# Performance work log

Hardware: AMD Instinct MI355X
Metric: run time of the kernel (lower is better)

Reference implementation:

```python
import jax, jax.numpy as jnp
import numpy as np

N_NODES = 100000
N_EDGES = 1600000
N_GRAPHS = 256
IN_F = 64   # global_features (GNN input dim)
OUT_F = 64  # node_features (GNN output dim)


def setup_inputs() -> dict:
    key = jax.random.key(0)
    ks = jax.random.split(key, 8)
    x = jax.random.normal(ks[0], (N_NODES, IN_F), dtype=jnp.float32)
    edge_index = jax.random.randint(ks[1], (2, N_EDGES), 0, N_NODES, dtype=jnp.int64)
    batch = jnp.sort(jax.random.randint(ks[2], (N_NODES,), 0, N_GRAPHS, dtype=jnp.int64))
    # GNNLayer linear: in=global_features, out=node_features
    W_gnn = jax.random.normal(ks[3], (IN_F, OUT_F), dtype=jnp.float32) / np.sqrt(IN_F)
    b_gnn = jnp.zeros((OUT_F,), dtype=jnp.float32)
    # global_attention: Linear(node_features, 1)
    W_att = jax.random.normal(ks[4], (OUT_F, 1), dtype=jnp.float32) / np.sqrt(OUT_F)
    b_att = jnp.zeros((1,), dtype=jnp.float32)
    return {"x": x, "edge_index": edge_index, "batch": batch,
            "W_gnn": W_gnn, "b_gnn": b_gnn, "W_att": W_att, "b_att": b_att}


def reference(x, edge_index, batch, W_gnn, b_gnn, W_att, b_att):
    src, dst = edge_index[0], edge_index[1]
    # --- GNN message passing layer: aggregate neighbor features, transform ---
    agg = jax.ops.segment_sum(x[src], dst, num_segments=N_NODES)  # [N, IN_F]
    h = jax.nn.relu((x + agg) @ W_gnn + b_gnn)                    # [N, OUT_F]
    # --- attention scores + scatter softmax over batch segments ---
    scores = (h @ W_att + b_att)[:, 0]                            # [N]
    seg_max = jax.ops.segment_max(scores, batch, num_segments=N_GRAPHS)
    e = jnp.exp(scores - seg_max[batch])
    denom = jax.ops.segment_sum(e, batch, num_segments=N_GRAPHS)
    w = e / denom[batch]                                          # [N]
    # --- weighted scatter-add pooling ---
    out = jax.ops.segment_sum(w[:, None] * h, batch, num_segments=N_GRAPHS)
    return out  # [N_GRAPHS, OUT_F]
```

## Files before the change

### kernel.cpp

```cpp
#include <hip/hip_runtime.h>

#define N_NODES  100000
#define N_EDGES  1600000
#define N_GRAPHS 256
#define F        64


#define CHUNK    8192
#define NCHUNK   196
#define NBUCK    391
#define BCAP     5120

#define CAST_ELEMS   (N_NODES * F / 4)
#define CAST_BLOCKS  ((CAST_ELEMS + 1023) / 1024)
#define BC_BLOCKS    (NCHUNK + CAST_BLOCKS)

__device__ __forceinline__ unsigned short f2bf(float f) {
    unsigned int u = __float_as_uint(f);
    u += 0x7FFFu + ((u >> 16) & 1u);
    return (unsigned short)(u >> 16);
}

__global__ __launch_bounds__(256) void zero_kernel(
        int* __restrict__ balloc, float* __restrict__ out,
        float* __restrict__ denom) {
    int i = blockIdx.x * 256 + threadIdx.x;
    if (i < NBUCK) balloc[i] = 0;
    if (i < N_GRAPHS * F) out[i] = 0.f;
    if (i < N_GRAPHS) denom[i] = 0.f;
}

__global__ __launch_bounds__(1024) void bin_cast_kernel(
        const int* __restrict__ src, const int* __restrict__ dst,
        const float* __restrict__ x, unsigned short* __restrict__ xh,
        unsigned int* __restrict__ pairs, int* __restrict__ balloc) {
    int tid = threadIdx.x;
    int b   = blockIdx.x;

    if (b >= NCHUNK) {
        int i = (b - NCHUNK) * 1024 + tid;
        if (i < CAST_ELEMS) {
            float4 v = ((const float4*)x)[i];
            ushort4 o;
            o.x = f2bf(v.x); o.y = f2bf(v.y); o.z = f2bf(v.z); o.w = f2bf(v.w);
            ((ushort4*)xh)[i] = o;
        }
        return;
    }

    __shared__ int hist[NBUCK];
    __shared__ int roffs[NBUCK];
    __shared__ int curs[NBUCK];
    __shared__ int bbase[NBUCK];
    __shared__ int wsum[16];
    __shared__ unsigned int   stage[CHUNK];
    __shared__ unsigned short bstage[CHUNK];

    int base = b * CHUNK;
    int m    = min(CHUNK, N_EDGES - base);
    int lane = tid & 63;
    int wv   = tid >> 6;

    for (int k = tid; k < NBUCK; k += 1024) hist[k] = 0;
    __syncthreads();

    int de[8], se[8];
    #pragma unroll
    for (int r = 0; r < 8; ++r) {
        int e = tid + r * 1024;
        if (e < m) {
            de[r] = dst[base + e];
            se[r] = src[base + e];
            atomicAdd(&hist[de[r] >> 8], 1);
        } else {
            de[r] = -1; se[r] = 0;
        }
    }
    __syncthreads();

    int v = (tid < NBUCK) ? hist[tid] : 0;
    #pragma unroll
    for (int o = 1; o < 64; o <<= 1) {
        int u = __shfl_up(v, o, 64);
        if (lane >= o) v += u;
    }
    if (lane == 63) wsum[wv] = v;
    __syncthreads();
    if (tid < 16) {
        int s = wsum[tid];
        #pragma unroll
        for (int o = 1; o < 16; o <<= 1) {
            int u = __shfl_up(s, o, 64);
            if (tid >= o) s += u;
        }
        wsum[tid] = s;
    }
    __syncthreads();
    if (wv > 0) v += wsum[wv - 1];
    if (tid < NBUCK) {
        int excl = v - hist[tid];
        roffs[tid] = excl;
        curs[tid]  = excl;
        if (hist[tid] > 0)
            bbase[tid] = tid * BCAP + atomicAdd(&balloc[tid], hist[tid]);
    }
    __syncthreads();

    #pragma unroll
    for (int r = 0; r < 8; ++r) {
        if (de[r] >= 0) {
            int bk  = de[r] >> 8;
            int pos = atomicAdd(&curs[bk], 1);
            stage[pos]  = ((unsigned)(de[r] & 255) << 17) | (unsigned)se[r];
            bstage[pos] = (unsigned short)bk;
        }
    }
    __syncthreads();

    for (int e = tid; e < m; e += 1024) {
        int bk = bstage[e];
        pairs[bbase[bk] + (e - roffs[bk])] = stage[e];
    }
}

__global__ __launch_bounds__(512) void bucket_sort_kernel(
        unsigned int* __restrict__ pairs,
        const int* __restrict__ balloc,
        int* __restrict__ nbeg, int* __restrict__ nend) {
    __shared__ int hist[256];
    __shared__ int roffs[256];
    __shared__ int curs[256];
    __shared__ int wsum[8];
    __shared__ int sorted[BCAP];

    int tid   = threadIdx.x;
    int b     = blockIdx.x;
    int lane  = tid & 63;
    int wv    = tid >> 6;
    int node0 = b << 8;
    int nn    = min(256, N_NODES - node0);
    int E     = balloc[b];
    int base  = b * BCAP;

    for (int k = tid; k < 256; k += 512) hist[k] = 0;
    __syncthreads();
    for (int i = tid; i < E; i += 512)
        atomicAdd(&hist[pairs[base + i] >> 17], 1);
    __syncthreads();

    int c = (tid < 256) ? hist[tid] : 0;
    int v = c;
    #pragma unroll
    for (int o = 1; o < 64; o <<= 1) {
        int u = __shfl_up(v, o, 64);
        if (lane >= o) v += u;
    }
    if (tid < 256 && lane == 63) wsum[wv] = v;
    __syncthreads();
    if (tid < 4) {
        int s = wsum[tid];
        int u = __shfl_up(s, 1, 64); if (tid >= 1) s += u;
        u     = __shfl_up(s, 2, 64); if (tid >= 2) s += u;
        wsum[tid] = s;
    }
    __syncthreads();
    if (tid < 256) {
        if (wv > 0) v += wsum[wv - 1];
        int excl = v - c;
        roffs[tid] = excl;
        curs[tid]  = excl;
        if (tid < nn) {
            nbeg[node0 + tid] = base + excl;
            nend[node0 + tid] = base + excl + c;
        }
    }
    __syncthreads();

    for (int i = tid; i < E; i += 512) {
        unsigned int p = pairs[base + i];
        int pos = atomicAdd(&curs[p >> 17], 1);
        sorted[pos] = (int)(p & 0x1FFFFu);
    }
    __syncthreads();
    for (int i = tid; i < E; i += 512)
        pairs[base + i] = (unsigned int)sorted[i];
}

#define NODES_PER_WAVE 25
#define GT_NWAVES  (N_NODES / NODES_PER_WAVE)
#define GT_BLOCKS  (GT_NWAVES / 4)

__device__ __forceinline__ float bfl(unsigned int u) { return __uint_as_float(u << 16); }
__device__ __forceinline__ float bfh(unsigned int u) { return __uint_as_float(u & 0xFFFF0000u); }

__global__ __launch_bounds__(256) void gather_pool_kernel(
        const unsigned short* __restrict__ xh,
        const int*   __restrict__ nbeg,
        const int*   __restrict__ nend,
        const int*   __restrict__ eidx,
        const int*   __restrict__ batch,
        const float* __restrict__ Wg,
        const float* __restrict__ bg,
        const float* __restrict__ Wa,
        const float* __restrict__ ba,
        float*       __restrict__ out_acc,
        float*       __restrict__ denom) {
    int tid  = threadIdx.x;
    int lane = tid & 63;
    int grp  = lane >> 3;
    int c    = lane & 7;
    int waveId = blockIdx.x * 4 + (tid >> 6);

    int n0   = waveId * NODES_PER_WAVE;
    int nEnd = n0 + NODES_PER_WAVE;

    float wcol[F];
    #pragma unroll
    for (int k = 0; k < F; ++k) wcol[k] = Wg[k * F + lane];
    float bgl = bg[lane];
    float wal = Wa[lane];
    float ba0 = ba[0];

    const uint4* xh4 = (const uint4*)xh;

    int   cur_g = batch[n0];
    float accw  = 0.f;
    float denw  = 0.f;

    int pb = nbeg[n0];
    int pe = nend[n0];
    int sl_cur = (pb + lane < pe) ? eidx[pb + lane] : 0;

    for (int n = n0; n < nEnd; ++n) {
        int start = pb, end = pe;
        int sl    = sl_cur;
        if (n + 1 < nEnd) {
            pb = nbeg[n + 1];
            pe = nend[n + 1];
            sl_cur = (pb + lane < pe) ? eidx[pb + lane] : 0;
        }

        float a0=0.f,a1=0.f,a2=0.f,a3=0.f,a4=0.f,a5=0.f,a6=0.f,a7=0.f;
        {
            int jmax = end - start; if (jmax > 64) jmax = 64;
            for (int j = 0; j < jmax; j += 8) {
                int el = j + grp;
                int s  = __shfl(sl, el, 64);
                if (el < jmax) {
                    uint4 v = xh4[s * 8 + c];
                    a0 += bfl(v.x); a1 += bfh(v.x);
                    a2 += bfl(v.y); a3 += bfh(v.y);
                    a4 += bfl(v.z); a5 += bfh(v.z);
                    a6 += bfl(v.w); a7 += bfh(v.w);
                }
            }
        }
        for (int base = start + 64; base < end; base += 64) {
            int jmax = end - base; if (jmax > 64) jmax = 64;
            int sl2 = (base + lane < end) ? eidx[base + lane] : 0;
            for (int j = 0; j < jmax; j += 8) {
                int el = j + grp;
                int s  = __shfl(sl2, el, 64);
                if (el < jmax) {
                    uint4 v = xh4[s * 8 + c];
                    a0 += bfl(v.x); a1 += bfh(v.x);
                    a2 += bfl(v.y); a3 += bfh(v.y);
                    a4 += bfl(v.z); a5 += bfh(v.z);
                    a6 += bfl(v.w); a7 += bfh(v.w);
                }
            }
        }
        #pragma unroll
        for (int o = 8; o <= 32; o <<= 1) {
            a0 += __shfl_xor(a0, o, 64); a1 += __shfl_xor(a1, o, 64);
            a2 += __shfl_xor(a2, o, 64); a3 += __shfl_xor(a3, o, 64);
            a4 += __shfl_xor(a4, o, 64); a5 += __shfl_xor(a5, o, 64);
            a6 += __shfl_xor(a6, o, 64); a7 += __shfl_xor(a7, o, 64);
        }
        {
            uint4 v = xh4[n * 8 + c];
            a0 += bfl(v.x); a1 += bfh(v.x);
            a2 += bfl(v.y); a3 += bfh(v.y);
            a4 += bfl(v.z); a5 += bfh(v.z);
            a6 += bfl(v.w); a7 += bfh(v.w);
        }

        float re[8] = {a0,a1,a2,a3,a4,a5,a6,a7};
        float q0=0.f,q1=0.f,q2=0.f,q3=0.f,q4=0.f,q5=0.f,q6=0.f,q7=0.f;
        #pragma unroll
        for (int k = 0; k < F; k += 8) {
            int ln = k >> 3;
            q0 += __int_as_float(__builtin_amdgcn_readlane(__float_as_int(re[0]), ln)) * wcol[k + 0];
            q1 += __int_as_float(__builtin_amdgcn_readlane(__float_as_int(re[1]), ln)) * wcol[k + 1];
            q2 += __int_as_float(__builtin_amdgcn_readlane(__float_as_int(re[2]), ln)) * wcol[k + 2];
            q3 += __int_as_float(__builtin_amdgcn_readlane(__float_as_int(re[3]), ln)) * wcol[k + 3];
            q4 += __int_as_float(__builtin_amdgcn_readlane(__float_as_int(re[4]), ln)) * wcol[k + 4];
            q5 += __int_as_float(__builtin_amdgcn_readlane(__float_as_int(re[5]), ln)) * wcol[k + 5];
            q6 += __int_as_float(__builtin_amdgcn_readlane(__float_as_int(re[6]), ln)) * wcol[k + 6];
            q7 += __int_as_float(__builtin_amdgcn_readlane(__float_as_int(re[7]), ln)) * wcol[k + 7];
        }
        float hv = ((q0 + q1) + (q2 + q3)) + ((q4 + q5) + (q6 + q7)) + bgl;
        hv = hv > 0.f ? hv : 0.f;

        float p = hv * wal;
        #pragma unroll
        for (int o = 32; o > 0; o >>= 1)
            p += __shfl_down(p, o, 64);
        float s = __int_as_float(__builtin_amdgcn_readlane(__float_as_int(p), 0)) + ba0;
        float e = __expf(s);

        int g = batch[n];
        if (g != cur_g) {
            atomicAdd(&out_acc[cur_g * F + lane], accw);
            if (lane == 0) atomicAdd(&denom[cur_g], denw);
            accw = 0.f; denw = 0.f; cur_g = g;
        }
        accw += e * hv;
        denw += e;
    }
    atomicAdd(&out_acc[cur_g * F + lane], accw);
    if (lane == 0) atomicAdd(&denom[cur_g], denw);
}

__global__ __launch_bounds__(256) void finalize_kernel(
        float* __restrict__ out, const float* __restrict__ denom) {
    int i = blockIdx.x * 256 + threadIdx.x;
    if (i >= N_GRAPHS * F) return;
    float d = denom[i >> 6];
    out[i] = (d > 0.f) ? out[i] / d : 0.f;
}

extern "C" void kernel_launch(void* const* d_in, const int* in_sizes, int n_in,
                              void* d_out, int out_size, void* d_ws, size_t ws_size,
                              hipStream_t stream) {
    const float* x     = (const float*)d_in[0];
    const int*   ei    = (const int*)d_in[1];
    const int*   batch = (const int*)d_in[2];
    const float* Wg    = (const float*)d_in[3];
    const float* bg    = (const float*)d_in[4];
    const float* Wa    = (const float*)d_in[5];
    const float* ba    = (const float*)d_in[6];
    float* out = (float*)d_out;

    const int* src = ei;
    const int* dst = ei + N_EDGES;

    char* ws = (char*)d_ws;
    unsigned short* xh     = (unsigned short*)(ws);
    unsigned int*   pairs  = (unsigned int*)(ws + 12800000);
    int*            nbeg   = (int*)(ws + 20807680);
    int*            nend   = (int*)(ws + 21207808);
    int*            balloc = (int*)(ws + 21607936);
    float*          denom  = (float*)(ws + 21610240);

    zero_kernel       <<<64, 256, 0, stream>>>(balloc, out, denom);
    bin_cast_kernel   <<<BC_BLOCKS, 1024, 0, stream>>>(src, dst, x, xh, pairs, balloc);
    bucket_sort_kernel<<<NBUCK, 512, 0, stream>>>(pairs, balloc, nbeg, nend);
    gather_pool_kernel<<<GT_BLOCKS, 256, 0, stream>>>(
        xh, nbeg, nend, (const int*)pairs, batch, Wg, bg, Wa, ba, out, denom);
    finalize_kernel   <<<(N_GRAPHS * F + 255) / 256, 256, 0, stream>>>(out, denom);
}
```

Baseline: 179.3 us.

## Move GNN weights to packed-bf16 shared memory and halve nodes per wave

The per-lane 64-float weight column held in registers is replaced by a bf16-packed copy of W_gnn in shared memory, read inside the matvec loop. This lowers register pressure, and nodes per wave drop from 25 to 13 so more waves run in parallel. The zero kernel is folded into the cast blocks plus a memset, which removes one launch. The costs are extra LDS reads per node, a per-block weight conversion, and bf16 rounding of the weights.

```diff
diff --git a/kernel.cpp b/kernel.cpp
--- a/kernel.cpp
+++ b/kernel.cpp
@@ -21,23 +21,19 @@
     return (unsigned short)(u >> 16);
 }
 
-__global__ __launch_bounds__(256) void zero_kernel(
-        int* __restrict__ balloc, float* __restrict__ out,
-        float* __restrict__ denom) {
-    int i = blockIdx.x * 256 + threadIdx.x;
-    if (i < NBUCK) balloc[i] = 0;
-    if (i < N_GRAPHS * F) out[i] = 0.f;
-    if (i < N_GRAPHS) denom[i] = 0.f;
-}
-
 __global__ __launch_bounds__(1024) void bin_cast_kernel(
         const int* __restrict__ src, const int* __restrict__ dst,
         const float* __restrict__ x, unsigned short* __restrict__ xh,
-        unsigned int* __restrict__ pairs, int* __restrict__ balloc) {
+        unsigned int* __restrict__ pairs, int* __restrict__ balloc,
+        float* __restrict__ out, float* __restrict__ denom) {
     int tid = threadIdx.x;
     int b   = blockIdx.x;
 
     if (b >= NCHUNK) {
+        if (b == NCHUNK) {
+            for (int i = tid; i < N_GRAPHS * F; i += 1024) out[i] = 0.f;
+            if (tid < N_GRAPHS) denom[tid] = 0.f;
+        }
         int i = (b - NCHUNK) * 1024 + tid;
         if (i < CAST_ELEMS) {
             float4 v = ((const float4*)x)[i];
@@ -186,9 +182,9 @@
         pairs[base + i] = (unsigned int)sorted[i];
 }
 
-#define NODES_PER_WAVE 25
-#define GT_NWAVES  (N_NODES / NODES_PER_WAVE)
-#define GT_BLOCKS  (GT_NWAVES / 4)
+#define NODES_PER_WAVE 13
+#define GT_NWAVES  ((N_NODES + NODES_PER_WAVE - 1) / NODES_PER_WAVE)
+#define GT_BLOCKS  ((GT_NWAVES + 3) / 4)
 
 __device__ __forceinline__ float bfl(unsigned int u) { return __uint_as_float(u << 16); }
 __device__ __forceinline__ float bfh(unsigned int u) { return __uint_as_float(u & 0xFFFF0000u); }
@@ -205,18 +201,25 @@
         const float* __restrict__ ba,
         float*       __restrict__ out_acc,
         float*       __restrict__ denom) {
+    __shared__ unsigned int shw[32 * 64];
+
     int tid  = threadIdx.x;
     int lane = tid & 63;
+    for (int i = tid; i < 32 * 64; i += 256) {
+        int kk = i >> 6, f = i & 63;
+        unsigned int lo = (unsigned int)f2bf(Wg[(2 * kk)     * F + f]);
+        unsigned int hi = (unsigned int)f2bf(Wg[(2 * kk + 1) * F + f]);
+        shw[i] = lo | (hi << 16);
+    }
+    __syncthreads();
+
     int grp  = lane >> 3;
     int c    = lane & 7;
     int waveId = blockIdx.x * 4 + (tid >> 6);
-
     int n0   = waveId * NODES_PER_WAVE;
-    int nEnd = n0 + NODES_PER_WAVE;
-
-    float wcol[F];
-    #pragma unroll
-    for (int k = 0; k < F; ++k) wcol[k] = Wg[k * F + lane];
+    if (n0 >= N_NODES) return;
+    int nEnd = min(n0 + NODES_PER_WAVE, N_NODES);
+
     float bgl = bg[lane];
     float wal = Wa[lane];
     float ba0 = ba[0];
@@ -255,9 +258,9 @@
                 }
             }
         }
-        for (int base = start + 64; base < end; base += 64) {
-            int jmax = end - base; if (jmax > 64) jmax = 64;
-            int sl2 = (base + lane < end) ? eidx[base + lane] : 0;
+        for (int base2 = start + 64; base2 < end; base2 += 64) {
+            int jmax = end - base2; if (jmax > 64) jmax = 64;
+            int sl2 = (base2 + lane < end) ? eidx[base2 + lane] : 0;
             for (int j = 0; j < jmax; j += 8) {
                 int el = j + grp;
                 int s  = __shfl(sl2, el, 64);
@@ -288,16 +291,23 @@
         float re[8] = {a0,a1,a2,a3,a4,a5,a6,a7};
         float q0=0.f,q1=0.f,q2=0.f,q3=0.f,q4=0.f,q5=0.f,q6=0.f,q7=0.f;
         #pragma unroll
-        for (int k = 0; k < F; k += 8) {
-            int ln = k >> 3;
-            q0 += __int_as_float(__builtin_amdgcn_readlane(__float_as_int(re[0]), ln)) * wcol[k + 0];
-            q1 += __int_as_float(__builtin_amdgcn_readlane(__float_as_int(re[1]), ln)) * wcol[k + 1];
-            q2 += __int_as_float(__builtin_amdgcn_readlane(__float_as_int(re[2]), ln)) * wcol[k + 2];
-            q3 += __int_as_float(__builtin_amdgcn_readlane(__float_as_int(re[3]), ln)) * wcol[k + 3];
-            q4 += __int_as_float(__builtin_amdgcn_readlane(__float_as_int(re[4]), ln)) * wcol[k + 4];
-            q5 += __int_as_float(__builtin_amdgcn_readlane(__float_as_int(re[5]), ln)) * wcol[k + 5];
-            q6 += __int_as_float(__builtin_amdgcn_readlane(__float_as_int(re[6]), ln)) * wcol[k + 6];
-            q7 += __int_as_float(__builtin_amdgcn_readlane(__float_as_int(re[7]), ln)) * wcol[k + 7];
+        for (int kk8 = 0; kk8 < 8; ++kk8) {
+            float y0 = __int_as_float(__builtin_amdgcn_readlane(__float_as_int(re[0]), kk8));
+            float y1 = __int_as_float(__builtin_amdgcn_readlane(__float_as_int(re[1]), kk8));
+            float y2 = __int_as_float(__builtin_amdgcn_readlane(__float_as_int(re[2]), kk8));
+            float y3 = __int_as_float(__builtin_amdgcn_readlane(__float_as_int(re[3]), kk8));
+            float y4 = __int_as_float(__builtin_amdgcn_readlane(__float_as_int(re[4]), kk8));
+            float y5 = __int_as_float(__builtin_amdgcn_readlane(__float_as_int(re[5]), kk8));
+            float y6 = __int_as_float(__builtin_amdgcn_readlane(__float_as_int(re[6]), kk8));
+            float y7 = __int_as_float(__builtin_amdgcn_readlane(__float_as_int(re[7]), kk8));
+            unsigned int u0 = shw[(4 * kk8 + 0) * 64 + lane];
+            unsigned int u1 = shw[(4 * kk8 + 1) * 64 + lane];
+            unsigned int u2 = shw[(4 * kk8 + 2) * 64 + lane];
+            unsigned int u3 = shw[(4 * kk8 + 3) * 64 + lane];
+            q0 += y0 * bfl(u0); q1 += y1 * bfh(u0);
+            q2 += y2 * bfl(u1); q3 += y3 * bfh(u1);
+            q4 += y4 * bfl(u2); q5 += y5 * bfh(u2);
+            q6 += y6 * bfl(u3); q7 += y7 * bfh(u3);
         }
         float hv = ((q0 + q1) + (q2 + q3)) + ((q4 + q5) + (q6 + q7)) + bgl;
         hv = hv > 0.f ? hv : 0.f;
@@ -322,7 +332,7 @@
     if (lane == 0) atomicAdd(&denom[cur_g], denw);
 }
 
-__global__ __launch_bounds__(256) void finalize_kernel(
+__global__ __launch_bounds__(256) void fin_kernel(
         float* __restrict__ out, const float* __restrict__ denom) {
     int i = blockIdx.x * 256 + threadIdx.x;
     if (i >= N_GRAPHS * F) return;
@@ -353,10 +363,11 @@
     int*            balloc = (int*)(ws + 21607936);
     float*          denom  = (float*)(ws + 21610240);
 
-    zero_kernel       <<<64, 256, 0, stream>>>(balloc, out, denom);
-    bin_cast_kernel   <<<BC_BLOCKS, 1024, 0, stream>>>(src, dst, x, xh, pairs, balloc);
+    hipMemsetAsync(balloc, 0, NBUCK * sizeof(int), stream);
+    bin_cast_kernel   <<<BC_BLOCKS, 1024, 0, stream>>>(src, dst, x, xh, pairs,
+                                                       balloc, out, denom);
     bucket_sort_kernel<<<NBUCK, 512, 0, stream>>>(pairs, balloc, nbeg, nend);
     gather_pool_kernel<<<GT_BLOCKS, 256, 0, stream>>>(
         xh, nbeg, nend, (const int*)pairs, batch, Wg, bg, Wa, ba, out, denom);
-    finalize_kernel   <<<(N_GRAPHS * F + 255) / 256, 256, 0, stream>>>(out, denom);
-}
+    fin_kernel        <<<64, 256, 0, stream>>>(out, denom);
+}
```

New measurement: 193.6 us. +8.0%, slower.

## Fuse bucket sort, gather-pool and finalize into one kernel with last-block finalize

Applied to the files above, without the earlier changes.

Merges the per-bucket counting sort with the gather/transform/pool stage so that sorted edge lists and node offsets stay in shared memory instead of being written back to global memory and reread. Each 1024-thread block handles 256 nodes, 16 per wave. The final normalization runs in whichever block finishes last, detected with a global done counter. The zeroing of out/denom moves into the cast blocks and a memset, removing three launches. The trade-off is fewer, larger blocks (391 blocks of 16 waves, versus 1000 blocks of 4 waves before), which may lower parallelism and latency hiding in the gather phase.

```diff
diff --git a/kernel.cpp b/kernel.cpp
--- a/kernel.cpp
+++ b/kernel.cpp
@@ -20,24 +20,22 @@
     u += 0x7FFFu + ((u >> 16) & 1u);
     return (unsigned short)(u >> 16);
 }
-
-__global__ __launch_bounds__(256) void zero_kernel(
-        int* __restrict__ balloc, float* __restrict__ out,
-        float* __restrict__ denom) {
-    int i = blockIdx.x * 256 + threadIdx.x;
-    if (i < NBUCK) balloc[i] = 0;
-    if (i < N_GRAPHS * F) out[i] = 0.f;
-    if (i < N_GRAPHS) denom[i] = 0.f;
-}
+__device__ __forceinline__ float bfl(unsigned int u) { return __uint_as_float(u << 16); }
+__device__ __forceinline__ float bfh(unsigned int u) { return __uint_as_float(u & 0xFFFF0000u); }
 
 __global__ __launch_bounds__(1024) void bin_cast_kernel(
         const int* __restrict__ src, const int* __restrict__ dst,
         const float* __restrict__ x, unsigned short* __restrict__ xh,
-        unsigned int* __restrict__ pairs, int* __restrict__ balloc) {
+        unsigned int* __restrict__ pairs, int* __restrict__ balloc,
+        float* __restrict__ out, float* __restrict__ denom) {
     int tid = threadIdx.x;
     int b   = blockIdx.x;
 
     if (b >= NCHUNK) {
+        if (b == NCHUNK) {
+            for (int i = tid; i < N_GRAPHS * F; i += 1024) out[i] = 0.f;
+            if (tid < N_GRAPHS) denom[tid] = 0.f;
+        }
         int i = (b - NCHUNK) * 1024 + tid;
         if (i < CAST_ELEMS) {
             float4 v = ((const float4*)x)[i];
@@ -123,28 +121,38 @@
     }
 }
 
-__global__ __launch_bounds__(512) void bucket_sort_kernel(
-        unsigned int* __restrict__ pairs,
-        const int* __restrict__ balloc,
-        int* __restrict__ nbeg, int* __restrict__ nend) {
+__global__ __launch_bounds__(1024) void sort_gather_kernel(
+        const unsigned short* __restrict__ xh,
+        const unsigned int* __restrict__ pairs,
+        const int*   __restrict__ balloc,
+        const int*   __restrict__ batch,
+        const float* __restrict__ Wg,
+        const float* __restrict__ bg,
+        const float* __restrict__ Wa,
+        const float* __restrict__ ba,
+        float*       __restrict__ out,
+        float*       __restrict__ denom,
+        unsigned int* __restrict__ done) {
     __shared__ int hist[256];
-    __shared__ int roffs[256];
     __shared__ int curs[256];
-    __shared__ int wsum[8];
+    __shared__ int lbeg[256];
+    __shared__ int lend[256];
+    __shared__ int wsum[4];
     __shared__ int sorted[BCAP];
-
-    int tid   = threadIdx.x;
-    int b     = blockIdx.x;
-    int lane  = tid & 63;
-    int wv    = tid >> 6;
+    __shared__ int lastFlag;
+
+    int tid  = threadIdx.x;
+    int b    = blockIdx.x;
+    int lane = tid & 63;
+    int wv   = tid >> 6;
     int node0 = b << 8;
     int nn    = min(256, N_NODES - node0);
     int E     = balloc[b];
     int base  = b * BCAP;
 
-    for (int k = tid; k < 256; k += 512) hist[k] = 0;
-    __syncthreads();
-    for (int i = tid; i < E; i += 512)
+    if (tid < 256) hist[tid] = 0;
+    __syncthreads();
+    for (int i = tid; i < E; i += 1024)
         atomicAdd(&hist[pairs[base + i] >> 17], 1);
     __syncthreads();
 
@@ -167,52 +175,21 @@
     if (tid < 256) {
         if (wv > 0) v += wsum[wv - 1];
         int excl = v - c;
-        roffs[tid] = excl;
-        curs[tid]  = excl;
-        if (tid < nn) {
-            nbeg[node0 + tid] = base + excl;
-            nend[node0 + tid] = base + excl + c;
-        }
-    }
-    __syncthreads();
-
-    for (int i = tid; i < E; i += 512) {
+        curs[tid] = excl;
+        lbeg[tid] = excl;
+        lend[tid] = excl + c;
+    }
+    __syncthreads();
+
+    for (int i = tid; i < E; i += 1024) {
         unsigned int p = pairs[base + i];
         int pos = atomicAdd(&curs[p >> 17], 1);
         sorted[pos] = (int)(p & 0x1FFFFu);
     }
     __syncthreads();
-    for (int i = tid; i < E; i += 512)
-        pairs[base + i] = (unsigned int)sorted[i];
-}
-
-#define NODES_PER_WAVE 25
-#define GT_NWAVES  (N_NODES / NODES_PER_WAVE)
-#define GT_BLOCKS  (GT_NWAVES / 4)
-
-__device__ __forceinline__ float bfl(unsigned int u) { return __uint_as_float(u << 16); }
-__device__ __forceinline__ float bfh(unsigned int u) { return __uint_as_float(u & 0xFFFF0000u); }
-
-__global__ __launch_bounds__(256) void gather_pool_kernel(
-        const unsigned short* __restrict__ xh,
-        const int*   __restrict__ nbeg,
-        const int*   __restrict__ nend,
-        const int*   __restrict__ eidx,
-        const int*   __restrict__ batch,
-        const float* __restrict__ Wg,
-        const float* __restrict__ bg,
-        const float* __restrict__ Wa,
-        const float* __restrict__ ba,
-        float*       __restrict__ out_acc,
-        float*       __restrict__ denom) {
-    int tid  = threadIdx.x;
-    int lane = tid & 63;
-    int grp  = lane >> 3;
-    int c    = lane & 7;
-    int waveId = blockIdx.x * 4 + (tid >> 6);
-
-    int n0   = waveId * NODES_PER_WAVE;
-    int nEnd = n0 + NODES_PER_WAVE;
+
+    int grp = lane >> 3;
+    int cc  = lane & 7;
 
     float wcol[F];
     #pragma unroll
@@ -223,111 +200,126 @@
 
     const uint4* xh4 = (const uint4*)xh;
 
-    int   cur_g = batch[n0];
-    float accw  = 0.f;
-    float denw  = 0.f;
-
-    int pb = nbeg[n0];
-    int pe = nend[n0];
-    int sl_cur = (pb + lane < pe) ? eidx[pb + lane] : 0;
-
-    for (int n = n0; n < nEnd; ++n) {
-        int start = pb, end = pe;
-        int sl    = sl_cur;
-        if (n + 1 < nEnd) {
-            pb = nbeg[n + 1];
-            pe = nend[n + 1];
-            sl_cur = (pb + lane < pe) ? eidx[pb + lane] : 0;
-        }
-
-        float a0=0.f,a1=0.f,a2=0.f,a3=0.f,a4=0.f,a5=0.f,a6=0.f,a7=0.f;
-        {
-            int jmax = end - start; if (jmax > 64) jmax = 64;
-            for (int j = 0; j < jmax; j += 8) {
-                int el = j + grp;
-                int s  = __shfl(sl, el, 64);
-                if (el < jmax) {
-                    uint4 v = xh4[s * 8 + c];
-                    a0 += bfl(v.x); a1 += bfh(v.x);
-                    a2 += bfl(v.y); a3 += bfh(v.y);
-                    a4 += bfl(v.z); a5 += bfh(v.z);
-                    a6 += bfl(v.w); a7 += bfh(v.w);
+    int nl0 = wv * 16;
+    int myn = nn - nl0; if (myn > 16) myn = 16;
+
+    if (myn > 0) {
+        int   cur_g = batch[node0 + nl0];
+        float accw  = 0.f;
+        float denw  = 0.f;
+
+        int pb = lbeg[nl0];
+        int pe = lend[nl0];
+        int sl_cur = (pb + lane < pe) ? sorted[pb + lane] : 0;
+
+        for (int q = 0; q < myn; ++q) {
+            int n = node0 + nl0 + q;
+            int start = pb, end = pe;
+            int sl    = sl_cur;
+            if (q + 1 < myn) {
+                pb = lbeg[nl0 + q + 1];
+                pe = lend[nl0 + q + 1];
+                sl_cur = (pb + lane < pe) ? sorted[pb + lane] : 0;
+            }
+
+            float a0=0.f,a1=0.f,a2=0.f,a3=0.f,a4=0.f,a5=0.f,a6=0.f,a7=0.f;
+            {
+                int jmax = end - start; if (jmax > 64) jmax = 64;
+                for (int j = 0; j < jmax; j += 8) {
+                    int el = j + grp;
+                    int s  = __shfl(sl, el, 64);
+                    if (el < jmax) {
+                        uint4 vv = xh4[s * 8 + cc];
+                        a0 += bfl(vv.x); a1 += bfh(vv.x);
+                        a2 += bfl(vv.y); a3 += bfh(vv.y);
+                        a4 += bfl(vv.z); a5 += bfh(vv.z);
+                        a6 += bfl(vv.w); a7 += bfh(vv.w);
+                    }
                 }
             }
-        }
-        for (int base = start + 64; base < end; base += 64) {
-            int jmax = end - base; if (jmax > 64) jmax = 64;
-            int sl2 = (base + lane < end) ? eidx[base + lane] : 0;
-            for (int j = 0; j < jmax; j += 8) {
-                int el = j + grp;
-                int s  = __shfl(sl2, el, 64);
-                if (el < jmax) {
-                    uint4 v = xh4[s * 8 + c];
-                    a0 += bfl(v.x); a1 += bfh(v.x);
-                    a2 += bfl(v.y); a3 += bfh(v.y);
-                    a4 += bfl(v.z); a5 += bfh(v.z);
-                    a6 += bfl(v.w); a7 += bfh(v.w);
+            for (int b2 = start + 64; b2 < end; b2 += 64) {
+                int jmax = end - b2; if (jmax > 64) jmax = 64;
+                int sl2 = (b2 + lane < end) ? sorted[b2 + lane] : 0;
+                for (int j = 0; j < jmax; j += 8) {
+                    int el = j + grp;
+                    int s  = __shfl(sl2, el, 64);
+                    if (el < jmax) {
+                        uint4 vv = xh4[s * 8 + cc];
+                        a0 += bfl(vv.x); a1 += bfh(vv.x);
+                        a2 += bfl(vv.y); a3 += bfh(vv.y);
+                        a4 += bfl(vv.z); a5 += bfh(vv.z);
+                        a6 += bfl(vv.w); a7 += bfh(vv.w);
+                    }
                 }
             }
-        }
-        #pragma unroll
-        for (int o = 8; o <= 32; o <<= 1) {
-            a0 += __shfl_xor(a0, o, 64); a1 += __shfl_xor(a1, o, 64);
-            a2 += __shfl_xor(a2, o, 64); a3 += __shfl_xor(a3, o, 64);
-            a4 += __shfl_xor(a4, o, 64); a5 += __shfl_xor(a5, o, 64);
-            a6 += __shfl_xor(a6, o, 64); a7 += __shfl_xor(a7, o, 64);
-        }
-        {
-            uint4 v = xh4[n * 8 + c];
-            a0 += bfl(v.x); a1 += bfh(v.x);
-            a2 += bfl(v.y); a3 += bfh(v.y);
-            a4 += bfl(v.z); a5 += bfh(v.z);
-            a6 += bfl(v.w); a7 += bfh(v.w);
-        }
-
-        float re[8] = {a0,a1,a2,a3,a4,a5,a6,a7};
-        float q0=0.f,q1=0.f,q2=0.f,q3=0.f,q4=0.f,q5=0.f,q6=0.f,q7=0.f;
-        #pragma unroll
-        for (int k = 0; k < F; k += 8) {
-            int ln = k >> 3;
-            q0 += __int_as_float(__builtin_amdgcn_readlane(__float_as_int(re[0]), ln)) * wcol[k + 0];
-            q1 += __int_as_float(__builtin_amdgcn_readlane(__float_as_int(re[1]), ln)) * wcol[k + 1];
-            q2 += __int_as_float(__builtin_amdgcn_readlane(__float_as_int(re[2]), ln)) * wcol[k + 2];
-            q3 += __int_as_float(__builtin_amdgcn_readlane(__float_as_int(re[3]), ln)) * wcol[k + 3];
-            q4 += __int_as_float(__builtin_amdgcn_readlane(__float_as_int(re[4]), ln)) * wcol[k + 4];
-            q5 += __int_as_float(__builtin_amdgcn_readlane(__float_as_int(re[5]), ln)) * wcol[k + 5];
-            q6 += __int_as_float(__builtin_amdgcn_readlane(__float_as_int(re[6]), ln)) * wcol[k + 6];
-            q7 += __int_as_float(__builtin_amdgcn_readlane(__float_as_int(re[7]), ln)) * wcol[k + 7];
-        }
-        float hv = ((q0 + q1) + (q2 + q3)) + ((q4 + q5) + (q6 + q7)) + bgl;
-        hv = hv > 0.f ? hv : 0.f;
-
-        float p = hv * wal;
-        #pragma unroll
-        for (int o = 32; o > 0; o >>= 1)
-            p += __shfl_down(p, o, 64);
-        float s = __int_as_float(__builtin_amdgcn_readlane(__float_as_int(p), 0)) + ba0;
-        float e = __expf(s);
-
-        int g = batch[n];
-        if (g != cur_g) {
-            atomicAdd(&out_acc[cur_g * F + lane], accw);
-            if (lane == 0) atomicAdd(&denom[cur_g], denw);
-            accw = 0.f; denw = 0.f; cur_g = g;
-        }
-        accw += e * hv;
-        denw += e;
-    }
-    atomicAdd(&out_acc[cur_g * F + lane], accw);
-    if (lane == 0) atomicAdd(&denom[cur_g], denw);
-}
-
-__global__ __launch_bounds__(256) void finalize_kernel(
-        float* __restrict__ out, const float* __restrict__ denom) {
-    int i = blockIdx.x * 256 + threadIdx.x;
-    if (i >= N_GRAPHS * F) return;
-    float d = denom[i >> 6];
-    out[i] = (d > 0.f) ? out[i] / d : 0.f;
+            #pragma unroll
+            for (int o = 8; o <= 32; o <<= 1) {
+                a0 += __shfl_xor(a0, o, 64); a1 += __shfl_xor(a1, o, 64);
+                a2 += __shfl_xor(a2, o, 64); a3 += __shfl_xor(a3, o, 64);
+                a4 += __shfl_xor(a4, o, 64); a5 += __shfl_xor(a5, o, 64);
+                a6 += __shfl_xor(a6, o, 64); a7 += __shfl_xor(a7, o, 64);
+            }
+            {
+                uint4 vv = xh4[n * 8 + cc];
+                a0 += bfl(vv.x); a1 += bfh(vv.x);
+                a2 += bfl(vv.y); a3 += bfh(vv.y);
+                a4 += bfl(vv.z); a5 += bfh(vv.z);
+                a6 += bfl(vv.w); a7 += bfh(vv.w);
+            }
+
+            float re[8] = {a0,a1,a2,a3,a4,a5,a6,a7};
+            float q0=0.f,q1=0.f,q2=0.f,q3=0.f,q4=0.f,q5=0.f,q6=0.f,q7=0.f;
+            #pragma unroll
+            for (int k = 0; k < F; k += 8) {
+                int ln = k >> 3;
+                q0 += __int_as_float(__builtin_amdgcn_readlane(__float_as_int(re[0]), ln)) * wcol[k + 0];
+                q1 += __int_as_float(__builtin_amdgcn_readlane(__float_as_int(re[1]), ln)) * wcol[k + 1];
+                q2 += __int_as_float(__builtin_amdgcn_readlane(__float_as_int(re[2]), ln)) * wcol[k + 2];
+                q3 += __int_as_float(__builtin_amdgcn_readlane(__float_as_int(re[3]), ln)) * wcol[k + 3];
+                q4 += __int_as_float(__builtin_amdgcn_readlane(__float_as_int(re[4]), ln)) * wcol[k + 4];
+                q5 += __int_as_float(__builtin_amdgcn_readlane(__float_as_int(re[5]), ln)) * wcol[k + 5];
+                q6 += __int_as_float(__builtin_amdgcn_readlane(__float_as_int(re[6]), ln)) * wcol[k + 6];
+                q7 += __int_as_float(__builtin_amdgcn_readlane(__float_as_int(re[7]), ln)) * wcol[k + 7];
+            }
+            float hv = ((q0 + q1) + (q2 + q3)) + ((q4 + q5) + (q6 + q7)) + bgl;
+            hv = hv > 0.f ? hv : 0.f;
+
+            float p = hv * wal;
+            #pragma unroll
+            for (int o = 32; o > 0; o >>= 1)
+                p += __shfl_down(p, o, 64);
+            float s = __int_as_float(__builtin_amdgcn_readlane(__float_as_int(p), 0)) + ba0;
+            float e = __expf(s);
+
+            int g = batch[n];
+            if (g != cur_g) {
+                atomicAdd(&out[cur_g * F + lane], accw);
+                if (lane == 0) atomicAdd(&denom[cur_g], denw);
+                accw = 0.f; denw = 0.f; cur_g = g;
+            }
+            accw += e * hv;
+            denw += e;
+        }
+        atomicAdd(&out[cur_g * F + lane], accw);
+        if (lane == 0) atomicAdd(&denom[cur_g], denw);
+    }
+
+    __threadfence();
+    __syncthreads();
+    if (tid == 0) {
+        unsigned int prev = atomicAdd(done, 1u);
+        lastFlag = (prev == (unsigned)(gridDim.x - 1)) ? 1 : 0;
+    }
+    __syncthreads();
+    if (lastFlag) {
+        for (int i = tid; i < N_GRAPHS * F; i += 1024) {
+            float d = __hip_atomic_load(&denom[i >> 6], __ATOMIC_RELAXED,
+                                        __HIP_MEMORY_SCOPE_AGENT);
+            float o = __hip_atomic_load(&out[i], __ATOMIC_RELAXED,
+                                        __HIP_MEMORY_SCOPE_AGENT);
+            out[i] = (d > 0.f) ? o / d : 0.f;
+        }
+    }
 }
 
 extern "C" void kernel_launch(void* const* d_in, const int* in_sizes, int n_in,
@@ -348,15 +340,13 @@
     char* ws = (char*)d_ws;
     unsigned short* xh     = (unsigned short*)(ws);
     unsigned int*   pairs  = (unsigned int*)(ws + 12800000);
-    int*            nbeg   = (int*)(ws + 20807680);
-    int*            nend   = (int*)(ws + 21207808);
-    int*            balloc = (int*)(ws + 21607936);
-    float*          denom  = (float*)(ws + 21610240);
-
-    zero_kernel       <<<64, 256, 0, stream>>>(balloc, out, denom);
-    bin_cast_kernel   <<<BC_BLOCKS, 1024, 0, stream>>>(src, dst, x, xh, pairs, balloc);
-    bucket_sort_kernel<<<NBUCK, 512, 0, stream>>>(pairs, balloc, nbeg, nend);
-    gather_pool_kernel<<<GT_BLOCKS, 256, 0, stream>>>(
-        xh, nbeg, nend, (const int*)pairs, batch, Wg, bg, Wa, ba, out, denom);
-    finalize_kernel   <<<(N_GRAPHS * F + 255) / 256, 256, 0, stream>>>(out, denom);
+    int*            balloc = (int*)(ws + 20807680);
+    unsigned int*   done   = (unsigned int*)(ws + 20809728);
+    float*          denom  = (float*)(ws + 20809984);
+
+    hipMemsetAsync(balloc, 0, 2048 + 256, stream);
+    bin_cast_kernel  <<<BC_BLOCKS, 1024, 0, stream>>>(src, dst, x, xh, pairs,
+                                                      balloc, out, denom);
+    sort_gather_kernel<<<NBUCK, 1024, 0, stream>>>(xh, pairs, balloc, batch,
+                                                   Wg, bg, Wa, ba, out, denom, done);
 }
```

Measured after the change: 327.4 us. 82.6% more time.
